# Performance work log

Measured on AMD Instinct MI355X. Metric: run time of the kernel, lower is better.

The kernel has to match this reference:

```python
import jax, jax.numpy as jnp
import numpy as np

C = 96
H = 4 * C  # hidden_channels = int(mlp_ratio * in_channels)
EPS = 1e-5  # torch LayerNorm default eps


def setup_inputs() -> dict:
    key = jax.random.key(0)
    ks = jax.random.split(key, 8)
    x = jax.random.normal(ks[0], (2, C, 64, 64, 64), dtype=jnp.float32)
    # depthwise conv3d: groups=C -> kernel (O=C, I/groups=1, 7,7,7)
    dw_w = jax.random.normal(ks[1], (C, 1, 7, 7, 7), dtype=jnp.float32) * 0.05
    dw_b = jax.random.normal(ks[2], (C,), dtype=jnp.float32) * 0.01
    ln_g = jnp.ones((C,), dtype=jnp.float32)
    ln_b = jnp.zeros((C,), dtype=jnp.float32)
    w1 = jax.random.normal(ks[3], (C, H), dtype=jnp.float32) * (1.0 / np.sqrt(C))
    b1 = jnp.zeros((H,), dtype=jnp.float32)
    w2 = jax.random.normal(ks[4], (H, C), dtype=jnp.float32) * (1.0 / np.sqrt(H))
    b2 = jnp.zeros((C,), dtype=jnp.float32)
    gamma = jnp.full((C,), 1e-6, dtype=jnp.float32)  # layer_scale init
    return {"x": x, "dw_w": dw_w, "dw_b": dw_b, "ln_g": ln_g, "ln_b": ln_b,
            "w1": w1, "b1": b1, "w2": w2, "b2": b2, "gamma": gamma}


def reference(x, dw_w, dw_b, ln_g, ln_b, w1, b1, w2, b2, gamma):
    # depthwise 3D conv, kernel 7, padding 3 (same), groups=C
    out = jax.lax.conv_general_dilated(
        x, dw_w, window_strides=(1, 1, 1), padding=[(3, 3)] * 3,
        dimension_numbers=("NCDHW", "OIDHW", "NCDHW"),
        feature_group_count=C)
    out = out + dw_b[None, :, None, None, None]
    # b c d h w -> b d h w c
    out = jnp.moveaxis(out, 1, -1)
    # LayerNorm over channel dim
    mu = jnp.mean(out, axis=-1, keepdims=True)
    var = jnp.mean(jnp.square(out - mu), axis=-1, keepdims=True)
    out = (out - mu) * jax.lax.rsqrt(var + EPS) * ln_g + ln_b
    # 2-layer MLP (pointwise convs as Linear), exact GELU like torch default
    out = jax.nn.gelu(out @ w1 + b1, approximate=False)
    out = out @ w2 + b2
    # layer scale
    out = gamma * out
    # b d h w c -> b c d h w, stochastic depth is identity (p=0), residual
    out = jnp.moveaxis(out, -1, 1)
    return out + x
```

## Files before the change

kernel.cpp:

```cpp
#include <hip/hip_runtime.h>

typedef unsigned int u32;
typedef unsigned short u16;
typedef unsigned long long u64;
typedef long i64;
typedef float f32x4 __attribute__((ext_vector_type(4)));
typedef u32 u32x4 __attribute__((ext_vector_type(4)));

__device__ __forceinline__ u16 f2bf_rne(float f) {
    return __builtin_bit_cast(u16, (__bf16)f);
}
__device__ __forceinline__ float bf2f(u16 h) {
    return __builtin_bit_cast(float, ((u32)h) << 16);
}
__device__ __forceinline__ float gelu_fast(float v) {
    float t = __builtin_amdgcn_exp2f(v * -2.4554673f);
    return v * __builtin_amdgcn_rcpf(1.f + t);
}
__device__ __forceinline__ i64 mk64(u32 lo, u32 hi) {
    return (i64)(((u64)hi << 32) | (u64)lo);
}
__device__ __forceinline__ u32 pk4(float a, float b, float c, float d) {
    u32 w = (u32)__builtin_amdgcn_cvt_pk_fp8_f32(a, b, 0, false);
    return (u32)__builtin_amdgcn_cvt_pk_fp8_f32(c, d, (int)w, true);
}

__global__ void prep_weights(const float* __restrict__ w1, const float* __restrict__ w2,
                             const float* __restrict__ lng, const float* __restrict__ lnb,
                             const float* __restrict__ b1,
                             i64* __restrict__ W1L, i64* __restrict__ W2L,
                             float* __restrict__ B1s) {
    int i = blockIdx.x * 256 + threadIdx.x;
    if (i < 4608) {
        int n16 = i / 192, r = i - n16 * 192;
        int kk = r >> 6, lane = r & 63;
        int n = n16 * 16 + (lane & 15);
        int cb = kk * 32 + (lane >> 4) * 8;
        float s0 = lng[cb + 0] * w1[(cb + 0) * 384 + n];
        float s1 = lng[cb + 1] * w1[(cb + 1) * 384 + n];
        float s2 = lng[cb + 2] * w1[(cb + 2) * 384 + n];
        float s3 = lng[cb + 3] * w1[(cb + 3) * 384 + n];
        float s4 = lng[cb + 4] * w1[(cb + 4) * 384 + n];
        float s5 = lng[cb + 5] * w1[(cb + 5) * 384 + n];
        float s6 = lng[cb + 6] * w1[(cb + 6) * 384 + n];
        float s7 = lng[cb + 7] * w1[(cb + 7) * 384 + n];
        W1L[i] = mk64(pk4(s0, s1, s2, s3), pk4(s4, s5, s6, s7));
    } else if (i < 9216) {
        int e = i - 4608;
        int r = e & 767, lane = r & 63, jk = r >> 6;
        int c = ((e / 768) * 16) + (lane & 15);
        int nb = jk * 32 + (lane >> 4) * 8;
        float s0 = w2[(nb + 0) * 96 + c], s1 = w2[(nb + 1) * 96 + c];
        float s2 = w2[(nb + 2) * 96 + c], s3 = w2[(nb + 3) * 96 + c];
        float s4 = w2[(nb + 4) * 96 + c], s5 = w2[(nb + 5) * 96 + c];
        float s6 = w2[(nb + 6) * 96 + c], s7 = w2[(nb + 7) * 96 + c];
        W2L[e] = mk64(pk4(s0, s1, s2, s3), pk4(s4, s5, s6, s7));
    } else if (i < 9600) {
        int n = i - 9216;
        float s = b1[n];
        for (int c = 0; c < 96; ++c) s += lnb[c] * w1[c * 384 + n];
        B1s[n] = s;
    }
}

__global__ void prep_bt(const float* __restrict__ dww, unsigned char* __restrict__ BT) {
    int i = blockIdx.x * 256 + threadIdx.x;
    if (i >= 301056) return;
    int lane = i & 63;
    int tap = (i >> 6) % 49;
    int c = i / 3136;
    int n = lane & 15, kg = lane >> 4;
    const float* wt = dww + c * 343 + tap * 7;
    float e[8];
#pragma unroll
    for (int j = 0; j < 8; ++j) {
        int t = kg * 8 + j - n;
        e[j] = (t >= 0 && t < 7) ? wt[t] : 0.f;
    }
    u32 lo = pk4(e[0], e[1], e[2], e[3]);
    u32 hi = pk4(e[4], e[5], e[6], e[7]);
    *(u32*)&BT[(size_t)i * 8] = lo;
    *(u32*)&BT[(size_t)i * 8 + 4] = hi;
}

template<int PACKED>
__global__ __launch_bounds__(512, 8) void dwconvM(const float* __restrict__ x,
                                                  const unsigned char* __restrict__ BT,
                                                  const float* __restrict__ dwb,
                                                  u16* __restrict__ cw16,
                                                  u16* __restrict__ o16) {
    __shared__ __align__(16) unsigned char tile[27104];
    const int tid = threadIdx.x;
    const int bx = blockIdx.x, c = blockIdx.y, b = blockIdx.z;
    const int d0 = (bx >> 2) * 8, h0 = (bx & 3) * 16;
    const float* xc = x + ((size_t)(b * 96 + c)) * 262144;

    for (int i = tid; i < 6160; i += 512) {
        int pz = i / 440;
        int rem = i - pz * 440;
        int row = rem / 20;
        int u = rem - row * 20;
        int d = d0 + pz - 3, h = h0 + row - 3;
        u32 pk = 0;
        if (((unsigned)d < 64u) && ((unsigned)h < 64u)) {
            const float* xr = xc + d * 4096 + h * 64;
            if (u >= 1 && u <= 15) {
                float e[4];
                __builtin_memcpy(e, xr + 4 * u - 3, 16);
                pk = pk4(e[0], e[1], e[2], e[3]);
            } else if (u == 0) {
                pk = pk4(0.f, 0.f, 0.f, xr[0]);
            } else if (u == 16) {
                pk = pk4(xr[61], xr[62], xr[63], 0.f);
            }
        }
        *(u32*)&tile[(pz * 22 + row) * 88 + u * 4] = pk;
    }
    __syncthreads();

    const int lane = tid & 63, wv = tid >> 6;
    const int n = lane & 15, g = lane >> 4;
    const unsigned char* BTl = BT + (size_t)c * 49 * 512 + (size_t)lane * 8;
    const int abase = n * 88 + 8 * g;

    f32x4 acc[4];
#pragma unroll
    for (int i = 0; i < 4; ++i) acc[i] = f32x4{0.f, 0.f, 0.f, 0.f};

    i64 bfC[7], bfN[7];
#pragma unroll
    for (int kh = 0; kh < 7; ++kh)
        bfC[kh] = *(const i64*)(BTl + (size_t)kh * 512);

#pragma unroll
    for (int kd = 0; kd < 7; ++kd) {
#pragma unroll
        for (int kh = 0; kh < 7; ++kh)
            bfN[kh] = (kd < 6) ? *(const i64*)(BTl + (size_t)((kd + 1) * 7 + kh) * 512)
                               : (i64)0;
        const unsigned char* tb = &tile[(wv + kd) * 1936 + abase];
#pragma unroll
        for (int kh = 0; kh < 7; ++kh) {
            const unsigned char* ab = tb + kh * 88;
#pragma unroll
            for (int wt = 0; wt < 4; ++wt) {
                i64 af = *(const i64*)(ab + 16 * wt);
                acc[wt] = __builtin_amdgcn_mfma_f32_16x16x32_fp8_fp8(af, bfC[kh], acc[wt], 0, 0, 0);
            }
        }
#pragma unroll
        for (int kh = 0; kh < 7; ++kh) bfC[kh] = bfN[kh];
    }

    const float bias = dwb[c];
    const int d = d0 + wv;
#pragma unroll
    for (int wt = 0; wt < 4; ++wt) {
#pragma unroll
        for (int q = 0; q < 4; ++q) {
            int h = h0 + 4 * g + q;
            int w = wt * 16 + n;
            u16 val = f2bf_rne(acc[wt][q] + bias);
            size_t pos = (size_t)b * 262144 + (size_t)d * 4096 + h * 64 + w;
            if (PACKED == 0)
                cw16[(size_t)c * 524288 + pos] = val;
            else
                o16[2 * ((size_t)(b * 96 + c) * 262144 + (size_t)d * 4096 + h * 64 + w) + 1] = val;
        }
    }
}

template<int PACKED>
__global__ __launch_bounds__(256, 5) void dwconvA(const float* __restrict__ x,
                                                  const float* __restrict__ dww,
                                                  const float* __restrict__ dwb,
                                                  u32* cw, u16* o16) {
    __shared__ u32 tile32[7920];
    const int tid = threadIdx.x;
    const int bx = blockIdx.x, c = blockIdx.y, b = blockIdx.z;
    const int d0 = (bx >> 2) * 4, h0 = (bx & 3) * 16;
    const float* xc = x + ((size_t)(b * 96 + c)) * 262144;

    for (int i = tid; i < 7700; i += 256) {
        int pz = i / 770;
        int rem = i - pz * 770;
        int r2 = rem / 70;
        int col = rem - r2 * 70;
        int d = d0 + pz - 3, h = h0 + 2 * r2 - 3, w = col - 3;
        float lo = 0.f, hi = 0.f;
        if (((unsigned)d < 64u) && ((unsigned)w < 64u)) {
            int base = d * 4096 + h * 64 + w;
            if ((unsigned)h < 64u) lo = xc[base];
            if ((unsigned)(h + 1) < 64u) hi = xc[base + 64];
        }
        int a = pz * 792 + r2 * 72 + col;
        int aw = ((((a >> 2) ^ ((a >> 5) & 1)) << 2)) | (a & 3);
        tile32[aw] = (u32)f2bf_rne(lo) | ((u32)f2bf_rne(hi) << 16);
    }
    __syncthreads();

    const int tx = tid & 7, ty = (tid >> 3) & 7, tz = tid >> 6;
    float a0[8], a1[8];
#pragma unroll
    for (int i = 0; i < 8; ++i) { a0[i] = 0.f; a1[i] = 0.f; }

    for (int kd = 0; kd < 7; ++kd) {
        const float* Wk = dww + c * 343 + kd * 49;
        const int pz = tz + kd;
#pragma unroll
        for (int pr = 0; pr < 4; ++pr) {
            const int g0 = pz * 198 + (ty + pr) * 18 + (tx << 1);
            u32 rb[16];
#pragma unroll
            for (int k = 0; k < 4; ++k) {
                int g = g0 + k;
                int ga = (g ^ ((g >> 3) & 1)) << 2;
                *(u32x4*)&rb[4 * k] = *(const u32x4*)(tile32 + ga);
            }
            float rlo[16], rhi[16];
#pragma unroll
            for (int t = 0; t < 16; ++t) {
                rlo[t] = __builtin_bit_cast(float, rb[t] << 16);
                rhi[t] = __builtin_bit_cast(float, rb[t]);
            }
#pragma unroll
            for (int kw = 0; kw < 7; ++kw) {
                float wA = Wk[2 * pr * 7 + kw];
#pragma unroll
                for (int i = 0; i < 8; ++i) {
                    a0[i] = fmaf(rlo[kw + i], wA, a0[i]);
                    a1[i] = fmaf(rhi[kw + i], wA, a1[i]);
                }
                if (pr < 3) {
                    float wB = Wk[(2 * pr + 1) * 7 + kw];
#pragma unroll
                    for (int i = 0; i < 8; ++i) a0[i] = fmaf(rhi[kw + i], wB, a0[i]);
                }
                if (pr > 0) {
                    float wC = Wk[(2 * pr - 1) * 7 + kw];
#pragma unroll
                    for (int i = 0; i < 8; ++i) a1[i] = fmaf(rlo[kw + i], wC, a1[i]);
                }
            }
        }
    }

    const float bias = dwb[c];
    const int d = d0 + tz;
    const int hA = h0 + 2 * ty;
    if (PACKED == 0) {
        const int p = b * 262144 + d * 4096 + hA * 64 + 8 * tx;
        u32* dst = cw + c * 262144 + (p >> 1);
#pragma unroll
        for (int k = 0; k < 4; ++k)
            dst[k] = (u32)f2bf_rne(a0[2 * k] + bias) | ((u32)f2bf_rne(a0[2 * k + 1] + bias) << 16);
        u32* dst1 = dst + 32;
#pragma unroll
        for (int k = 0; k < 4; ++k)
            dst1[k] = (u32)f2bf_rne(a1[2 * k] + bias) | ((u32)f2bf_rne(a1[2 * k + 1] + bias) << 16);
    } else {
        size_t e = ((size_t)(b * 96 + c)) * 262144 + d * 4096 + hA * 64 + 8 * tx;
#pragma unroll
        for (int i = 0; i < 8; ++i) o16[2 * (e + i) + 1] = f2bf_rne(a0[i] + bias);
#pragma unroll
        for (int i = 0; i < 8; ++i) o16[2 * (e + 64 + i) + 1] = f2bf_rne(a1[i] + bias);
    }
}

template<int CWP, int WF>
__global__ __launch_bounds__(256, 4) void mlp3(const void* cwsrc,
                                               const i64* __restrict__ W1L,
                                               const i64* __restrict__ W2L,
                                               const float* __restrict__ B1s,
                                               const float* __restrict__ w1f,
                                               const float* __restrict__ w2f,
                                               const float* __restrict__ lng,
                                               const float* __restrict__ lnb,
                                               const float* __restrict__ b1g,
                                               const float* __restrict__ b2g,
                                               const float* __restrict__ gam,
                                               const float* __restrict__ x,
                                               float* __restrict__ out) {
    __shared__ __align__(16) unsigned char HS[4][2][1152];

    const int tid = threadIdx.x;
    const int wv = tid >> 6, lane = tid & 63;
    const int p = lane & 15, G = lane >> 4;
    const int pos0 = blockIdx.x * 128 + wv * 32;
    const int b = pos0 >> 18, prel0 = pos0 & 262143;
    unsigned char* hsw = &HS[wv][0][0];

    i64 aF[2][3];
#pragma unroll
    for (int t = 0; t < 2; ++t) {
        float v[3][8];
        if (CWP == 0) {
            const u16* cw16 = (const u16*)cwsrc;
#pragma unroll
            for (int kk = 0; kk < 3; ++kk)
#pragma unroll
                for (int m = 0; m < 8; ++m) {
                    int c = kk * 32 + G * 8 + m;
                    v[kk][m] = bf2f(cw16[(size_t)c * 524288 + pos0 + t * 16 + p]);
                }
        } else {
            const u32* ow = (const u32*)cwsrc;
#pragma unroll
            for (int kk = 0; kk < 3; ++kk)
#pragma unroll
                for (int m = 0; m < 8; ++m) {
                    int c = kk * 32 + G * 8 + m;
                    v[kk][m] = bf2f((u16)(ow[((size_t)(b * 96 + c)) * 262144 + prel0 + t * 16 + p] >> 16));
                }
        }
        float s = 0.f, sq = 0.f;
#pragma unroll
        for (int kk = 0; kk < 3; ++kk)
#pragma unroll
            for (int m = 0; m < 8; ++m) { s += v[kk][m]; sq += v[kk][m] * v[kk][m]; }
        s += __shfl_xor(s, 16); sq += __shfl_xor(sq, 16);
        s += __shfl_xor(s, 32); sq += __shfl_xor(sq, 32);
        float mu = s * (1.f / 96.f);
        float rstd = rsqrtf(sq * (1.f / 96.f) - mu * mu + 1e-5f);
#pragma unroll
        for (int kk = 0; kk < 3; ++kk) {
            float n0 = (v[kk][0] - mu) * rstd, n1 = (v[kk][1] - mu) * rstd;
            float n2 = (v[kk][2] - mu) * rstd, n3 = (v[kk][3] - mu) * rstd;
            float n4 = (v[kk][4] - mu) * rstd, n5 = (v[kk][5] - mu) * rstd;
            float n6 = (v[kk][6] - mu) * rstd, n7 = (v[kk][7] - mu) * rstd;
            aF[t][kk] = mk64(pk4(n0, n1, n2, n3), pk4(n4, n5, n6, n7));
        }
    }

    f32x4 acc[2][6];
#pragma unroll
    for (int t = 0; t < 2; ++t)
#pragma unroll
        for (int i = 0; i < 6; ++i) acc[t][i] = f32x4{0.f, 0.f, 0.f, 0.f};

    for (int j = 0; j < 6; ++j) {
        i64 wf[12];
#pragma unroll
        for (int q = 0; q < 12; ++q) {
            if (WF == 0) {
                wf[q] = W1L[(j * 12 + q) * 64 + lane];
            } else {
                int nt = q / 3, kk = q - nt * 3;
                int nn = (j * 4 + nt) * 16 + p;
                int cb = kk * 32 + G * 8;
                wf[q] = mk64(
                    pk4(lng[cb + 0] * w1f[(cb + 0) * 384 + nn], lng[cb + 1] * w1f[(cb + 1) * 384 + nn],
                        lng[cb + 2] * w1f[(cb + 2) * 384 + nn], lng[cb + 3] * w1f[(cb + 3) * 384 + nn]),
                    pk4(lng[cb + 4] * w1f[(cb + 4) * 384 + nn], lng[cb + 5] * w1f[(cb + 5) * 384 + nn],
                        lng[cb + 6] * w1f[(cb + 6) * 384 + nn], lng[cb + 7] * w1f[(cb + 7) * 384 + nn]));
            }
        }
        f32x4 bb[4];
#pragma unroll
        for (int nt = 0; nt < 4; ++nt)
            bb[nt] = *(const f32x4*)&B1s[(j * 4 + nt) * 16 + 4 * G];

#pragma unroll
        for (int t = 0; t < 2; ++t) {
            f32x4 c1[4];
#pragma unroll
            for (int nt = 0; nt < 4; ++nt) {
                c1[nt] = f32x4{0.f, 0.f, 0.f, 0.f};
#pragma unroll
                for (int kk = 0; kk < 3; ++kk)
                    c1[nt] = __builtin_amdgcn_mfma_f32_16x16x32_fp8_fp8(wf[nt * 3 + kk], aF[t][kk], c1[nt], 0, 0, 0);
            }
#pragma unroll
            for (int nt = 0; nt < 4; ++nt) {
                float g0 = gelu_fast(c1[nt][0] + bb[nt][0]);
                float g1 = gelu_fast(c1[nt][1] + bb[nt][1]);
                float g2 = gelu_fast(c1[nt][2] + bb[nt][2]);
                float g3 = gelu_fast(c1[nt][3] + bb[nt][3]);
                *(u32*)&hsw[t * 1152 + p * 72 + nt * 16 + 4 * G] = pk4(g0, g1, g2, g3);
            }
        }

        i64 w2r[12];
#pragma unroll
        for (int q = 0; q < 12; ++q) {
            int ct = q >> 1, kkj = q & 1;
            if (WF == 0) {
                w2r[q] = W2L[(ct * 12 + j * 2 + kkj) * 64 + lane];
            } else {
                int cc = ct * 16 + p;
                int nb = (j * 2 + kkj) * 32 + G * 8;
                w2r[q] = mk64(
                    pk4(w2f[(nb + 0) * 96 + cc], w2f[(nb + 1) * 96 + cc],
                        w2f[(nb + 2) * 96 + cc], w2f[(nb + 3) * 96 + cc]),
                    pk4(w2f[(nb + 4) * 96 + cc], w2f[(nb + 5) * 96 + cc],
                        w2f[(nb + 6) * 96 + cc], w2f[(nb + 7) * 96 + cc]));
            }
        }

        asm volatile("s_waitcnt lgkmcnt(0)" ::: "memory");
        __builtin_amdgcn_sched_barrier(0);

        i64 hF[2][2];
#pragma unroll
        for (int t = 0; t < 2; ++t)
#pragma unroll
            for (int kkj = 0; kkj < 2; ++kkj)
                hF[t][kkj] = *(const i64*)&hsw[t * 1152 + p * 72 + kkj * 32 + G * 8];

#pragma unroll
        for (int ct = 0; ct < 6; ++ct)
#pragma unroll
            for (int kkj = 0; kkj < 2; ++kkj) {
#pragma unroll
                for (int t = 0; t < 2; ++t)
                    acc[t][ct] = __builtin_amdgcn_mfma_f32_16x16x32_fp8_fp8(hF[t][kkj], w2r[ct * 2 + kkj], acc[t][ct], 0, 0, 0);
            }
    }

#pragma unroll
    for (int ct = 0; ct < 6; ++ct) {
        int c = ct * 16 + p;
        float b2c = b2g[c], gc = gam[c];
#pragma unroll
        for (int t = 0; t < 2; ++t) {
            size_t xi = ((size_t)(b * 96 + c)) * 262144 + prel0 + t * 16 + G * 4;
            f32x4 xv = *(const f32x4*)&x[xi];
            f32x4 o;
#pragma unroll
            for (int r = 0; r < 4; ++r) o[r] = (acc[t][ct][r] + b2c) * gc + xv[r];
            *(f32x4*)&out[xi] = o;
        }
    }
}

extern "C" void kernel_launch(void* const* d_in, const int* in_sizes, int n_in,
                              void* d_out, int out_size, void* d_ws, size_t ws_size,
                              hipStream_t stream) {
    const float* x   = (const float*)d_in[0];
    const float* dww = (const float*)d_in[1];
    const float* dwb = (const float*)d_in[2];
    const float* lng = (const float*)d_in[3];
    const float* lnb = (const float*)d_in[4];
    const float* w1  = (const float*)d_in[5];
    const float* b1  = (const float*)d_in[6];
    const float* w2  = (const float*)d_in[7];
    const float* b2  = (const float*)d_in[8];
    const float* gam = (const float*)d_in[9];
    float* out = (float*)d_out;

    const size_t NEED_W  = 75264;
    const size_t NEED_BT = 75264 + 2408448ull;
    const size_t NEED_FULL = NEED_BT + 100663296ull;
    const bool wsW  = ws_size >= NEED_W;
    const bool wsBT = ws_size >= NEED_BT;
    const bool wsCW = ws_size >= NEED_FULL;

    i64* W1L = (i64*)d_ws;
    i64* W2L = (i64*)((char*)d_ws + 36864);
    float* B1s = (float*)((char*)d_ws + 73728);
    unsigned char* BT = (unsigned char*)d_ws + 75264;
    u32* cw = (u32*)((char*)d_ws + 2483712);

    if (wsW)
        hipLaunchKernelGGL(prep_weights, dim3(38), dim3(256), 0, stream,
                           w1, w2, lng, lnb, b1, W1L, W2L, B1s);
    if (wsBT)
        hipLaunchKernelGGL(prep_bt, dim3(1176), dim3(256), 0, stream, dww, BT);

    dim3 g1(32, 96, 2), blkc(512);
    if (wsCW)
        hipLaunchKernelGGL((dwconvM<0>), g1, blkc, 0, stream, x, BT, dwb, (u16*)cw, (u16*)d_out);
    else if (wsBT)
        hipLaunchKernelGGL((dwconvM<1>), g1, blkc, 0, stream, x, BT, dwb, (u16*)cw, (u16*)d_out);
    else {
        dim3 g1a(64, 96, 2), blka(256);
        hipLaunchKernelGGL((dwconvA<1>), g1a, blka, 0, stream, x, dww, dwb, cw, (u16*)d_out);
    }

    dim3 g2(4096), blk2(256);
    if (wsCW)
        hipLaunchKernelGGL((mlp3<0, 0>), g2, blk2, 0, stream, (const void*)cw,
                           W1L, W2L, B1s, w1, w2, lng, lnb, b1, b2, gam, x, out);
    else if (wsW)
        hipLaunchKernelGGL((mlp3<1, 0>), g2, blk2, 0, stream, (const void*)d_out,
                           W1L, W2L, B1s, w1, w2, lng, lnb, b1, b2, gam, x, out);
    else
        hipLaunchKernelGGL((mlp3<1, 1>), g2, blk2, 0, stream, (const void*)d_out,
                           W1L, W2L, B1s, w1, w2, lng, lnb, b1, b2, gam, x, out);
}
```

Measured before the change: 398.7 us.

## Process 16 depth planes per conv block and pair positions in MLP loads

Each depthwise-conv block now stages 22 padded planes in LDS and computes two output planes per wave, covering 16 depth planes instead of 8. This cuts the redundant halo loads of x per output. The conv is also split into one launch per batch. The MLP kernel assigns two adjacent positions per lane, so the bf16 intermediate is read as 32-bit words and the residual is read and written as float2. The larger LDS tile lowers the number of resident conv blocks, and the extra launch adds overhead.

```diff
diff --git a/kernel.cpp b/kernel.cpp
--- a/kernel.cpp
+++ b/kernel.cpp
@@ -5,6 +5,7 @@
 typedef unsigned long long u64;
 typedef long i64;
 typedef float f32x4 __attribute__((ext_vector_type(4)));
+typedef float f32x2 __attribute__((ext_vector_type(2)));
 typedef u32 u32x4 __attribute__((ext_vector_type(4)));
 
 __device__ __forceinline__ u16 f2bf_rne(float f) {
@@ -88,14 +89,14 @@
                                                   const unsigned char* __restrict__ BT,
                                                   const float* __restrict__ dwb,
                                                   u16* __restrict__ cw16,
-                                                  u16* __restrict__ o16) {
-    __shared__ __align__(16) unsigned char tile[27104];
+                                                  u16* __restrict__ o16, int b) {
+    __shared__ __align__(16) unsigned char tile[42592];
     const int tid = threadIdx.x;
-    const int bx = blockIdx.x, c = blockIdx.y, b = blockIdx.z;
-    const int d0 = (bx >> 2) * 8, h0 = (bx & 3) * 16;
+    const int bx = blockIdx.x, c = blockIdx.y;
+    const int d0 = (bx >> 2) * 16, h0 = (bx & 3) * 16;
     const float* xc = x + ((size_t)(b * 96 + c)) * 262144;
 
-    for (int i = tid; i < 6160; i += 512) {
+    for (int i = tid; i < 9680; i += 512) {
         int pz = i / 440;
         int rem = i - pz * 440;
         int row = rem / 20;
@@ -122,50 +123,55 @@
     const int n = lane & 15, g = lane >> 4;
     const unsigned char* BTl = BT + (size_t)c * 49 * 512 + (size_t)lane * 8;
     const int abase = n * 88 + 8 * g;
-
-    f32x4 acc[4];
-#pragma unroll
-    for (int i = 0; i < 4; ++i) acc[i] = f32x4{0.f, 0.f, 0.f, 0.f};
-
-    i64 bfC[7], bfN[7];
-#pragma unroll
-    for (int kh = 0; kh < 7; ++kh)
-        bfC[kh] = *(const i64*)(BTl + (size_t)kh * 512);
-
-#pragma unroll
-    for (int kd = 0; kd < 7; ++kd) {
+    const float bias = dwb[c];
+
+#pragma unroll
+    for (int plane = 0; plane < 2; ++plane) {
+        const int dd = wv + plane * 8;
+
+        f32x4 acc[4];
+#pragma unroll
+        for (int i = 0; i < 4; ++i) acc[i] = f32x4{0.f, 0.f, 0.f, 0.f};
+
+        i64 bfC[7], bfN[7];
 #pragma unroll
         for (int kh = 0; kh < 7; ++kh)
-            bfN[kh] = (kd < 6) ? *(const i64*)(BTl + (size_t)((kd + 1) * 7 + kh) * 512)
-                               : (i64)0;
-        const unsigned char* tb = &tile[(wv + kd) * 1936 + abase];
-#pragma unroll
-        for (int kh = 0; kh < 7; ++kh) {
-            const unsigned char* ab = tb + kh * 88;
-#pragma unroll
-            for (int wt = 0; wt < 4; ++wt) {
-                i64 af = *(const i64*)(ab + 16 * wt);
-                acc[wt] = __builtin_amdgcn_mfma_f32_16x16x32_fp8_fp8(af, bfC[kh], acc[wt], 0, 0, 0);
-            }
-        }
-#pragma unroll
-        for (int kh = 0; kh < 7; ++kh) bfC[kh] = bfN[kh];
-    }
-
-    const float bias = dwb[c];
-    const int d = d0 + wv;
-#pragma unroll
-    for (int wt = 0; wt < 4; ++wt) {
-#pragma unroll
-        for (int q = 0; q < 4; ++q) {
-            int h = h0 + 4 * g + q;
-            int w = wt * 16 + n;
-            u16 val = f2bf_rne(acc[wt][q] + bias);
-            size_t pos = (size_t)b * 262144 + (size_t)d * 4096 + h * 64 + w;
-            if (PACKED == 0)
-                cw16[(size_t)c * 524288 + pos] = val;
-            else
-                o16[2 * ((size_t)(b * 96 + c) * 262144 + (size_t)d * 4096 + h * 64 + w) + 1] = val;
+            bfC[kh] = *(const i64*)(BTl + (size_t)kh * 512);
+
+#pragma unroll
+        for (int kd = 0; kd < 7; ++kd) {
+#pragma unroll
+            for (int kh = 0; kh < 7; ++kh)
+                bfN[kh] = (kd < 6) ? *(const i64*)(BTl + (size_t)((kd + 1) * 7 + kh) * 512)
+                                   : (i64)0;
+            const unsigned char* tb = &tile[(dd + kd) * 1936 + abase];
+#pragma unroll
+            for (int kh = 0; kh < 7; ++kh) {
+                const unsigned char* ab = tb + kh * 88;
+#pragma unroll
+                for (int wt = 0; wt < 4; ++wt) {
+                    i64 af = *(const i64*)(ab + 16 * wt);
+                    acc[wt] = __builtin_amdgcn_mfma_f32_16x16x32_fp8_fp8(af, bfC[kh], acc[wt], 0, 0, 0);
+                }
+            }
+#pragma unroll
+            for (int kh = 0; kh < 7; ++kh) bfC[kh] = bfN[kh];
+        }
+
+        const int d = d0 + dd;
+#pragma unroll
+        for (int wt = 0; wt < 4; ++wt) {
+#pragma unroll
+            for (int q = 0; q < 4; ++q) {
+                int h = h0 + 4 * g + q;
+                int w = wt * 16 + n;
+                u16 val = f2bf_rne(acc[wt][q] + bias);
+                size_t pos = (size_t)b * 262144 + (size_t)d * 4096 + h * 64 + w;
+                if (PACKED == 0)
+                    cw16[(size_t)c * 524288 + pos] = val;
+                else
+                    o16[2 * ((size_t)(b * 96 + c) * 262144 + (size_t)d * 4096 + h * 64 + w) + 1] = val;
+            }
         }
     }
 }
@@ -290,46 +296,61 @@
     const int b = pos0 >> 18, prel0 = pos0 & 262143;
     unsigned char* hsw = &HS[wv][0][0];
 
+    float v0[3][8], v1[3][8];
+    if (CWP == 0) {
+        const u32* cw32 = (const u32*)cwsrc;
+#pragma unroll
+        for (int kk = 0; kk < 3; ++kk)
+#pragma unroll
+            for (int m = 0; m < 8; ++m) {
+                int c = kk * 32 + G * 8 + m;
+                u32 pr = cw32[(size_t)c * 262144 + (pos0 >> 1) + p];
+                v0[kk][m] = bf2f((u16)(pr & 0xffffu));
+                v1[kk][m] = bf2f((u16)(pr >> 16));
+            }
+    } else {
+        const u32* ow = (const u32*)cwsrc;
+#pragma unroll
+        for (int kk = 0; kk < 3; ++kk)
+#pragma unroll
+            for (int m = 0; m < 8; ++m) {
+                int c = kk * 32 + G * 8 + m;
+                size_t base = ((size_t)(b * 96 + c)) * 262144 + prel0 + 2 * p;
+                v0[kk][m] = bf2f((u16)(ow[base] >> 16));
+                v1[kk][m] = bf2f((u16)(ow[base + 1] >> 16));
+            }
+    }
+
+    float s0 = 0.f, sq0 = 0.f, s1 = 0.f, sq1 = 0.f;
+#pragma unroll
+    for (int kk = 0; kk < 3; ++kk)
+#pragma unroll
+        for (int m = 0; m < 8; ++m) {
+            s0 += v0[kk][m]; sq0 += v0[kk][m] * v0[kk][m];
+            s1 += v1[kk][m]; sq1 += v1[kk][m] * v1[kk][m];
+        }
+    s0 += __shfl_xor(s0, 16); sq0 += __shfl_xor(sq0, 16);
+    s0 += __shfl_xor(s0, 32); sq0 += __shfl_xor(sq0, 32);
+    s1 += __shfl_xor(s1, 16); sq1 += __shfl_xor(sq1, 16);
+    s1 += __shfl_xor(s1, 32); sq1 += __shfl_xor(sq1, 32);
+    float mu0 = s0 * (1.f / 96.f);
+    float rstd0 = rsqrtf(sq0 * (1.f / 96.f) - mu0 * mu0 + 1e-5f);
+    float mu1 = s1 * (1.f / 96.f);
+    float rstd1 = rsqrtf(sq1 * (1.f / 96.f) - mu1 * mu1 + 1e-5f);
+
     i64 aF[2][3];
 #pragma unroll
-    for (int t = 0; t < 2; ++t) {
-        float v[3][8];
-        if (CWP == 0) {
-            const u16* cw16 = (const u16*)cwsrc;
-#pragma unroll
-            for (int kk = 0; kk < 3; ++kk)
-#pragma unroll
-                for (int m = 0; m < 8; ++m) {
-                    int c = kk * 32 + G * 8 + m;
-                    v[kk][m] = bf2f(cw16[(size_t)c * 524288 + pos0 + t * 16 + p]);
-                }
-        } else {
-            const u32* ow = (const u32*)cwsrc;
-#pragma unroll
-            for (int kk = 0; kk < 3; ++kk)
-#pragma unroll
-                for (int m = 0; m < 8; ++m) {
-                    int c = kk * 32 + G * 8 + m;
-                    v[kk][m] = bf2f((u16)(ow[((size_t)(b * 96 + c)) * 262144 + prel0 + t * 16 + p] >> 16));
-                }
-        }
-        float s = 0.f, sq = 0.f;
-#pragma unroll
-        for (int kk = 0; kk < 3; ++kk)
-#pragma unroll
-            for (int m = 0; m < 8; ++m) { s += v[kk][m]; sq += v[kk][m] * v[kk][m]; }
-        s += __shfl_xor(s, 16); sq += __shfl_xor(sq, 16);
-        s += __shfl_xor(s, 32); sq += __shfl_xor(sq, 32);
-        float mu = s * (1.f / 96.f);
-        float rstd = rsqrtf(sq * (1.f / 96.f) - mu * mu + 1e-5f);
-#pragma unroll
-        for (int kk = 0; kk < 3; ++kk) {
-            float n0 = (v[kk][0] - mu) * rstd, n1 = (v[kk][1] - mu) * rstd;
-            float n2 = (v[kk][2] - mu) * rstd, n3 = (v[kk][3] - mu) * rstd;
-            float n4 = (v[kk][4] - mu) * rstd, n5 = (v[kk][5] - mu) * rstd;
-            float n6 = (v[kk][6] - mu) * rstd, n7 = (v[kk][7] - mu) * rstd;
-            aF[t][kk] = mk64(pk4(n0, n1, n2, n3), pk4(n4, n5, n6, n7));
-        }
+    for (int kk = 0; kk < 3; ++kk) {
+        aF[0][kk] = mk64(
+            pk4((v0[kk][0] - mu0) * rstd0, (v0[kk][1] - mu0) * rstd0,
+                (v0[kk][2] - mu0) * rstd0, (v0[kk][3] - mu0) * rstd0),
+            pk4((v0[kk][4] - mu0) * rstd0, (v0[kk][5] - mu0) * rstd0,
+                (v0[kk][6] - mu0) * rstd0, (v0[kk][7] - mu0) * rstd0));
+        aF[1][kk] = mk64(
+            pk4((v1[kk][0] - mu1) * rstd1, (v1[kk][1] - mu1) * rstd1,
+                (v1[kk][2] - mu1) * rstd1, (v1[kk][3] - mu1) * rstd1),
+            pk4((v1[kk][4] - mu1) * rstd1, (v1[kk][5] - mu1) * rstd1,
+                (v1[kk][6] - mu1) * rstd1, (v1[kk][7] - mu1) * rstd1));
     }
 
     f32x4 acc[2][6];
@@ -422,13 +443,13 @@
         int c = ct * 16 + p;
         float b2c = b2g[c], gc = gam[c];
 #pragma unroll
-        for (int t = 0; t < 2; ++t) {
-            size_t xi = ((size_t)(b * 96 + c)) * 262144 + prel0 + t * 16 + G * 4;
-            f32x4 xv = *(const f32x4*)&x[xi];
-            f32x4 o;
-#pragma unroll
-            for (int r = 0; r < 4; ++r) o[r] = (acc[t][ct][r] + b2c) * gc + xv[r];
-            *(f32x4*)&out[xi] = o;
+        for (int r = 0; r < 4; ++r) {
+            size_t xi = ((size_t)(b * 96 + c)) * 262144 + prel0 + 8 * G + 2 * r;
+            f32x2 xv = *(const f32x2*)&x[xi];
+            f32x2 o;
+            o[0] = (acc[0][ct][r] + b2c) * gc + xv[0];
+            o[1] = (acc[1][ct][r] + b2c) * gc + xv[1];
+            *(f32x2*)&out[xi] = o;
         }
     }
 }
@@ -467,12 +488,14 @@
     if (wsBT)
         hipLaunchKernelGGL(prep_bt, dim3(1176), dim3(256), 0, stream, dww, BT);
 
-    dim3 g1(32, 96, 2), blkc(512);
-    if (wsCW)
-        hipLaunchKernelGGL((dwconvM<0>), g1, blkc, 0, stream, x, BT, dwb, (u16*)cw, (u16*)d_out);
-    else if (wsBT)
-        hipLaunchKernelGGL((dwconvM<1>), g1, blkc, 0, stream, x, BT, dwb, (u16*)cw, (u16*)d_out);
-    else {
+    dim3 g1(16, 96, 1), blkc(512);
+    if (wsCW) {
+        hipLaunchKernelGGL((dwconvM<0>), g1, blkc, 0, stream, x, BT, dwb, (u16*)cw, (u16*)d_out, 0);
+        hipLaunchKernelGGL((dwconvM<0>), g1, blkc, 0, stream, x, BT, dwb, (u16*)cw, (u16*)d_out, 1);
+    } else if (wsBT) {
+        hipLaunchKernelGGL((dwconvM<1>), g1, blkc, 0, stream, x, BT, dwb, (u16*)cw, (u16*)d_out, 0);
+        hipLaunchKernelGGL((dwconvM<1>), g1, blkc, 0, stream, x, BT, dwb, (u16*)cw, (u16*)d_out, 1);
+    } else {
         dim3 g1a(64, 96, 2), blka(256);
         hipLaunchKernelGGL((dwconvA<1>), g1a, blka, 0, stream, x, dww, dwb, cw, (u16*)d_out);
     }
```

After: 395.8 us. Within noise of the previous version (-0.7%).
